# Optimization experiments

Hardware: AMD Instinct MI355X
Metric: run time of the kernel (lower is better)

Reference implementation:

```python
import jax, jax.numpy as jnp
import numpy as np

B, S, D, H = 2, 2048, 1024, 16
DK = D // H  # 64
ROPE_THETA = 10000.0


def apply_rope(t, positions):
    # t: [B, H, S, DK]; positions: [B, S]
    half = DK // 2
    inv_freq = 1.0 / (ROPE_THETA ** (jnp.arange(0, DK, 2, dtype=jnp.float32) / DK))  # [half]
    ang = positions.astype(jnp.float32)[:, None, :, None] * inv_freq  # [B,1,S,half]
    cos, sin = jnp.cos(ang), jnp.sin(ang)
    t_even = t[..., 0::2]
    t_odd = t[..., 1::2]
    r_even = t_even * cos - t_odd * sin
    r_odd = t_even * sin + t_odd * cos
    # interleave back to original layout
    return jnp.stack([r_even, r_odd], axis=-1).reshape(t.shape)


def setup_inputs() -> dict:
    key = jax.random.key(0)
    ks = jax.random.split(key, 5)
    x = jax.random.normal(ks[0], (B, S, D), dtype=jnp.float32)
    token_positions = jnp.broadcast_to(jnp.arange(S, dtype=jnp.int64 if jax.config.jax_enable_x64 else jnp.int32), (B, S))
    w_q = jax.random.normal(ks[1], (D, D), dtype=jnp.float32)
    w_k = jax.random.normal(ks[2], (D, D), dtype=jnp.float32)
    w_v = jax.random.normal(ks[3], (D, D), dtype=jnp.float32)
    w_o = jax.random.normal(ks[4], (D, D), dtype=jnp.float32)
    return {"x": x, "token_positions": token_positions, "w_q": w_q, "w_k": w_k, "w_v": w_v, "w_o": w_o}


def reference(x, token_positions, w_q, w_k, w_v, w_o):
    # project: weights stored as (h*d_k, d_model)
    wq = w_q.reshape(H, DK, D)
    wk = w_k.reshape(H, DK, D)
    wv = w_v.reshape(H, DK, D)
    q = jnp.einsum('bsd,hkd->bhsk', x, wq)  # [B,H,S,DK]
    k = jnp.einsum('bsd,hkd->bhsk', x, wk)
    v = jnp.einsum('bsd,hkd->bhsk', x, wv)
    q = apply_rope(q, token_positions)
    k = apply_rope(k, token_positions)
    scale = 1.0 / jnp.sqrt(jnp.float32(DK))
    scores = jnp.einsum('bhnk,bhmk->bhnm', q, k) * scale  # [B,H,S,S]
    causal = jnp.tril(jnp.ones((S, S), dtype=bool))
    scores = jnp.where(causal, scores, -jnp.inf)
    attn = jax.nn.softmax(scores, axis=-1)
    out = jnp.einsum('bhnm,bhmv->bhnv', attn, v)  # [B,H,S,DK]
    out = jnp.transpose(out, (0, 2, 1, 3)).reshape(B, S, H * DK)
    return jnp.einsum('bsf,df->bsd', out, w_o)
```

## Files before the change

### kernel.cpp

```cpp
#include <hip/hip_runtime.h>

typedef unsigned short u16;
typedef unsigned int u32;
typedef __attribute__((ext_vector_type(8))) __bf16 bf16x8;
typedef __attribute__((ext_vector_type(4))) float f32x4;

#define NSEQ 2048
#define NDIM 1024
#define NHEAD 16
#define NTOK 4096
#define NX   4194304
#define NWEL 1048576

__device__ __forceinline__ u16 f2bf(float f) {
  unsigned u = __float_as_uint(f);
  return (u16)((u + 0x7fffu + ((u >> 16) & 1u)) >> 16);
}
__device__ __forceinline__ float bf2f(u16 h) {
  return __uint_as_float(((unsigned)h) << 16);
}
__device__ __forceinline__ bf16x8 ld16(const u16* p) {
  int4 v = *reinterpret_cast<const int4*>(p);
  return __builtin_bit_cast(bf16x8, v);
}
__device__ __forceinline__ f32x4 mfma16(bf16x8 a, bf16x8 b, f32x4 c) {
  return __builtin_amdgcn_mfma_f32_16x16x32_bf16(a, b, c, 0, 0, 0);
}
__device__ __forceinline__ void gload16(const u16* g, u16* l) {
  __builtin_amdgcn_global_load_lds(
      (const __attribute__((address_space(1))) void*)g,
      (__attribute__((address_space(3))) void*)l, 16, 0, 0);
}

#define GEMM_PROLOGUE                                                         \
  const int tid = threadIdx.x;                                                \
  const int lane = tid & 63, wid = tid >> 6;                                  \
  const int wm = wid >> 1, wn = wid & 1;                                      \
  const int lr = lane & 15, lg = lane >> 4;                                   \
  const int srow_ = tid >> 2;                                                 \
  const int sch_ = ((tid & 3) ^ ((tid >> 3) & 3)) * 8;                        \
  const int rsw_ = (lg ^ ((lr >> 1) & 3)) * 8;

#define STAGE3(BB, AH, AL, BH, BL, T0, J0, K0)                                \
  {                                                                           \
    u16* bb_ = (BB);                                                          \
    gload16(AH + (size_t)((T0) + srow_) * NDIM + (K0) + sch_, bb_ + tid * 8); \
    gload16(AH + (size_t)((T0) + 64 + srow_) * NDIM + (K0) + sch_,            \
            bb_ + 2048 + tid * 8);                                            \
    gload16(BH + (size_t)((J0) + srow_) * NDIM + (K0) + sch_,                 \
            bb_ + 4096 + tid * 8);                                            \
    gload16(BH + (size_t)((J0) + 64 + srow_) * NDIM + (K0) + sch_,            \
            bb_ + 6144 + tid * 8);                                            \
    gload16(AL + (size_t)((T0) + srow_) * NDIM + (K0) + sch_,                 \
            bb_ + 8192 + tid * 8);                                            \
    gload16(AL + (size_t)((T0) + 64 + srow_) * NDIM + (K0) + sch_,            \
            bb_ + 10240 + tid * 8);                                           \
    gload16(BL + (size_t)((J0) + srow_) * NDIM + (K0) + sch_,                 \
            bb_ + 12288 + tid * 8);                                           \
    gload16(BL + (size_t)((J0) + 64 + srow_) * NDIM + (K0) + sch_,            \
            bb_ + 14336 + tid * 8);                                           \
  }

#define GEMM3_LOOP(AH, AL, BH, BL, T0, J0)                                    \
  STAGE3(lds, AH, AL, BH, BL, T0, J0, 0)                                      \
  __syncthreads();                                                            \
  for (int k0 = 0; k0 < NDIM; k0 += 32) {                                     \
    u16* cb_ = lds + ((k0 >> 5) & 1) * 16384;                                 \
    if (k0 + 32 < NDIM) {                                                     \
      u16* nb_ = lds + ((((k0 >> 5) & 1) ^ 1) * 16384);                       \
      STAGE3(nb_, AH, AL, BH, BL, T0, J0, k0 + 32)                            \
    }                                                                         \
    bf16x8 afh[4], afl[4];                                                    \
    _Pragma("unroll") for (int m = 0; m < 4; m++) {                           \
      int off = (wm * 64 + m * 16 + lr) * 32 + rsw_;                          \
      afh[m] = ld16(cb_ + off);                                               \
      afl[m] = ld16(cb_ + 8192 + off);                                        \
    }                                                                         \
    _Pragma("unroll") for (int n = 0; n < 4; n++) {                           \
      int off = (wn * 64 + n * 16 + lr) * 32 + rsw_;                          \
      bf16x8 bfh = ld16(cb_ + 4096 + off);                                    \
      bf16x8 bfl = ld16(cb_ + 12288 + off);                                   \
      _Pragma("unroll") for (int m = 0; m < 4; m++) {                         \
        acc[m][n] = mfma16(afh[m], bfh, acc[m][n]);                           \
        acc[m][n] = mfma16(afh[m], bfl, acc[m][n]);                           \
        acc[m][n] = mfma16(afl[m], bfh, acc[m][n]);                           \
      }                                                                       \
    }                                                                         \
    __syncthreads();                                                          \
  }

#define STAGE1(BB, AH, BH, T0, J0, K0)                                        \
  {                                                                           \
    u16* bb_ = (BB);                                                          \
    gload16(AH + (size_t)((T0) + srow_) * NDIM + (K0) + sch_, bb_ + tid * 8); \
    gload16(AH + (size_t)((T0) + 64 + srow_) * NDIM + (K0) + sch_,            \
            bb_ + 2048 + tid * 8);                                            \
    gload16(BH + (size_t)((J0) + srow_) * NDIM + (K0) + sch_,                 \
            bb_ + 4096 + tid * 8);                                            \
    gload16(BH + (size_t)((J0) + 64 + srow_) * NDIM + (K0) + sch_,            \
            bb_ + 6144 + tid * 8);                                            \
  }

#define GEMM1_LOOP(AH, BH, T0, J0)                                            \
  STAGE1(lds, AH, BH, T0, J0, 0)                                              \
  __syncthreads();                                                            \
  for (int k0 = 0; k0 < NDIM; k0 += 32) {                                     \
    u16* cb_ = lds + ((k0 >> 5) & 1) * 8192;                                  \
    if (k0 + 32 < NDIM) {                                                     \
      u16* nb_ = lds + ((((k0 >> 5) & 1) ^ 1) * 8192);                        \
      STAGE1(nb_, AH, BH, T0, J0, k0 + 32)                                    \
    }                                                                         \
    bf16x8 afh[4];                                                            \
    _Pragma("unroll") for (int m = 0; m < 4; m++) {                           \
      int off = (wm * 64 + m * 16 + lr) * 32 + rsw_;                          \
      afh[m] = ld16(cb_ + off);                                               \
    }                                                                         \
    _Pragma("unroll") for (int n = 0; n < 4; n++) {                           \
      int off = (wn * 64 + n * 16 + lr) * 32 + rsw_;                          \
      bf16x8 bfh = ld16(cb_ + 4096 + off);                                    \
      _Pragma("unroll") for (int m = 0; m < 4; m++) {                         \
        acc[m][n] = mfma16(afh[m], bfh, acc[m][n]);                           \
      }                                                                       \
    }                                                                         \
    __syncthreads();                                                          \
  }

__global__ __launch_bounds__(256) void k_prep(
    const float* __restrict__ x, const float* __restrict__ wq,
    const float* __restrict__ wk, const float* __restrict__ wv,
    const float* __restrict__ wo,
    u16* __restrict__ xh, u16* __restrict__ xl,
    u16* __restrict__ wh, u16* __restrict__ wl) {
  int g = blockIdx.x * 256 + threadIdx.x;
  const float4* src;
  u16 *dh, *dl;
  int idx;
  bool wantlo = true;
  if (g < NX / 4) {
    src = (const float4*)x; dh = xh; dl = xl; idx = g;
  } else {
    int z = (g - NX / 4) / (NWEL / 4);
    int r = (g - NX / 4) % (NWEL / 4);
    src = (const float4*)(z == 0 ? wq : z == 1 ? wk : z == 2 ? wv : wo);
    dh = wh + (size_t)z * NWEL; dl = wl + (size_t)z * NWEL; idx = r;
    wantlo = (z < 2);
  }
  float4 v = src[idx];
  u16 h0 = f2bf(v.x), h1 = f2bf(v.y), h2 = f2bf(v.z), h3 = f2bf(v.w);
  ushort4 hv = make_ushort4(h0, h1, h2, h3);
  ((ushort4*)dh)[idx] = hv;
  if (wantlo) {
    ushort4 lv = make_ushort4(f2bf(v.x - bf2f(h0)), f2bf(v.y - bf2f(h1)),
                              f2bf(v.z - bf2f(h2)), f2bf(v.w - bf2f(h3)));
    ((ushort4*)dl)[idx] = lv;
  }
}

__global__ __launch_bounds__(256) void k_tab(float2* __restrict__ csn) {
  int idx = blockIdx.x * 256 + threadIdx.x;
  int p = idx >> 5, j = idx & 31;
  double invf = exp((double)(2 * j) * (-9.210340371976184 / 64.0));
  double ang = (double)p * invf;
  double kq = rint(ang * 0.15915494309189535);
  float a = (float)(ang - kq * 6.283185307179586);
  csn[idx] = make_float2(cosf(a), sinf(a));
}

__global__ __launch_bounds__(256) void k_qkv(
    const u16* __restrict__ xh, const u16* __restrict__ xl,
    const u16* __restrict__ wh, const u16* __restrict__ wl,
    const int* __restrict__ tokpos, const float2* __restrict__ csn,
    u16* __restrict__ qh, u16* __restrict__ ql,
    u16* __restrict__ kh, u16* __restrict__ kl) {
  __shared__ __align__(16) u16 lds[32768];
  const int z = blockIdx.z;
  const int t0 = blockIdx.y * 128, j0 = blockIdx.x * 128;
  const int h0 = j0 >> 6;
  GEMM_PROLOGUE
  const u16* Bh = wh + (size_t)z * NWEL;
  const u16* Bl = wl + (size_t)z * NWEL;
  f32x4 acc[4][4];
#pragma unroll
  for (int m = 0; m < 4; m++)
#pragma unroll
    for (int n = 0; n < 4; n++) acc[m][n] = f32x4{0.f, 0.f, 0.f, 0.f};
  GEMM3_LOOP(xh, xl, Bh, Bl, t0, j0)

  const int b = t0 >> 11, s0 = t0 & 2047;
  u16* dh = (z == 0) ? qh : kh;
  u16* dl = (z == 0) ? ql : kl;
  float rv[4][4][4];
#pragma unroll
  for (int m = 0; m < 4; m++) {
#pragma unroll
    for (int r = 0; r < 4; r++) {
      int pos = tokpos[t0 + wm * 64 + m * 16 + lg * 4 + r];
#pragma unroll
      for (int n = 0; n < 4; n++) {
        float val = acc[m][n][r];
        float nb = __shfl_xor(val, 1);
        int dk = (wn * 64 + n * 16 + lr) & 63;
        float2 cs = csn[pos * 32 + (dk >> 1)];
        rv[m][r][n] = (dk & 1) ? (nb * cs.y + val * cs.x)
                               : (val * cs.x - nb * cs.y);
      }
    }
  }
#pragma unroll
  for (int pass = 0; pass < 2; pass++) {
    __syncthreads();
#pragma unroll
    for (int m = 0; m < 4; m++)
#pragma unroll
      for (int r = 0; r < 4; r++) {
        int rloc = wm * 64 + m * 16 + lg * 4 + r;
#pragma unroll
        for (int n = 0; n < 4; n++) {
          int cloc = wn * 64 + n * 16 + lr;
          float v = rv[m][r][n];
          u16 hi = f2bf(v);
          lds[rloc * 128 + cloc] = pass == 0 ? hi : f2bf(v - bf2f(hi));
        }
      }
    __syncthreads();
    u16* dst = pass == 0 ? dh : dl;
#pragma unroll
    for (int i = 0; i < 8; i++) {
      int idx = tid + i * 256;
      int r = idx >> 4, cc = idx & 15;
      int4 v = *(int4*)(lds + r * 128 + cc * 8);
      int h2 = cc >> 3, dk = (cc & 7) * 8;
      size_t off = ((size_t)((b * NHEAD + h0 + h2) * NSEQ + s0 + r)) * 64 + dk;
      *(int4*)(dst + off) = v;
    }
  }
}

__global__ __launch_bounds__(256) void k_v(
    const u16* __restrict__ xh, const u16* __restrict__ wvh,
    u16* __restrict__ vt) {
  __shared__ __align__(16) u16 lds[16384];
  const int t0 = blockIdx.y * 128, j0 = blockIdx.x * 128;
  const int h0 = j0 >> 6;
  GEMM_PROLOGUE
  f32x4 acc[4][4];
#pragma unroll
  for (int m = 0; m < 4; m++)
#pragma unroll
    for (int n = 0; n < 4; n++) acc[m][n] = f32x4{0.f, 0.f, 0.f, 0.f};
  GEMM1_LOOP(xh, wvh, t0, j0)
  const int b = t0 >> 11, s0 = t0 & 2047;
#pragma unroll
  for (int m = 0; m < 4; m++)
#pragma unroll
    for (int r = 0; r < 4; r++) {
      int rloc = wm * 64 + m * 16 + lg * 4 + r;
#pragma unroll
      for (int n = 0; n < 4; n++) {
        int cloc = wn * 64 + n * 16 + lr;
        lds[cloc * 128 + (rloc ^ ((cloc & 15) << 3))] = f2bf(acc[m][n][r]);
      }
    }
  __syncthreads();
#pragma unroll
  for (int i = 0; i < 8; i++) {
    int idx = tid + i * 256;
    int col = idx >> 4, rc = idx & 15;
    int4 v = *(int4*)(lds + col * 128 + ((rc * 8) ^ ((col & 15) << 3)));
    int h2 = col >> 6, dk = col & 63;
    size_t off = ((size_t)((b * NHEAD + h0 + h2) * 64 + dk)) * NSEQ + s0 + rc * 8;
    *(int4*)(vt + off) = v;
  }
}

#define ATT_STAGE(SEL, KT)                                                    \
  _Pragma("unroll") for (int j_ = 0; j_ < 6; j_++) {                          \
    int seg_ = w * 6 + j_;                                                    \
    int ten_ = seg_ >> 3, sub_ = seg_ & 7;                                    \
    int row_ = sub_ * 8 + (lane >> 3);                                        \
    int sc_ = ((lane & 7) * 8) ^ ((row_ & 7) * 8);             \
    u16* dst_ = (ten_ == 0 ? &skh[SEL][0]                                     \
                           : ten_ == 1 ? &skl[SEL][0] : &svb[SEL][0]) +       \
                sub_ * 512;                                                   \
    const u16* src_ =                                                         \
        (ten_ == 2)                                                           \
            ? vt + vbase + (size_t)row_ * NSEQ + (KT) * 64 + sc_              \
            : (ten_ == 0 ? kh : kl) + base + (size_t)((KT) * 64 + row_) * 64 + sc_; \
    gload16(src_, dst_);                                                      \
  }

__global__ __launch_bounds__(256) void k_attn(
    const u16* __restrict__ qh, const u16* __restrict__ ql,
    const u16* __restrict__ kh, const u16* __restrict__ kl,
    const u16* __restrict__ vt, u16* __restrict__ ah) {
  __shared__ __align__(16) u16 skh[2][4096];
  __shared__ __align__(16) u16 skl[2][4096];
  __shared__ __align__(16) u16 svb[2][4096];
  __shared__ __align__(16) u16 sp[4096];
  const int tid = threadIdx.x, lane = tid & 63, w = tid >> 6;
  const int lr = lane & 15, lg = lane >> 4;
  const int bh = blockIdx.y;
  const size_t base = (size_t)bh * NSEQ * 64;
  const size_t vbase = (size_t)bh * 64 * NSEQ;
  const int b = bh >> 4, h = bh & 15;
  const int qbA = 31 - blockIdx.x, qbB = blockIdx.x;

  for (int ph = 0; ph < 2; ph++) {
    const int qblk = ph ? qbB : qbA;
    const int q0 = qblk * 64;
    const int nt = qblk + 1;
    const int qrow_g = q0 + w * 16 + lr;
    bf16x8 qfh[2], qfl[2];
#pragma unroll
    for (int kk = 0; kk < 2; kk++) {
      qfh[kk] = ld16(qh + base + (size_t)qrow_g * 64 + kk * 32 + lg * 8);
      qfl[kk] = ld16(ql + base + (size_t)qrow_g * 64 + kk * 32 + lg * 8);
    }
    float mrun = -__builtin_inff(), lrun = 0.f;
    f32x4 oacc[4];
#pragma unroll
    for (int nf = 0; nf < 4; nf++) oacc[nf] = f32x4{0.f, 0.f, 0.f, 0.f};

    int sel = 0;
    ATT_STAGE(0, 0)
    __syncthreads();
    for (int kt = 0; kt < nt; kt++) {
      if (kt + 1 < nt) { ATT_STAGE(sel ^ 1, kt + 1) }
      f32x4 sacc[4];
#pragma unroll
      for (int nf = 0; nf < 4; nf++) sacc[nf] = f32x4{0.f, 0.f, 0.f, 0.f};
#pragma unroll
      for (int nf = 0; nf < 4; nf++) {
        int krow = nf * 16 + lr;
        int swz = (krow & 7) * 8;
#pragma unroll
        for (int kk = 0; kk < 2; kk++) {
          int off = krow * 64 + ((kk * 32 + lg * 8) ^ swz);
          bf16x8 kfh = ld16(&skh[sel][0] + off);
          bf16x8 kfl = ld16(&skl[sel][0] + off);
          sacc[nf] = mfma16(kfh, qfh[kk], sacc[nf]);
          sacc[nf] = mfma16(kfl, qfh[kk], sacc[nf]);
          sacc[nf] = mfma16(kfh, qfl[kk], sacc[nf]);
        }
      }
      float sv[4][4];
      float mm[4];
#pragma unroll
      for (int nf = 0; nf < 4; nf++) {
#pragma unroll
        for (int r = 0; r < 4; r++) sv[nf][r] = sacc[nf][r] * 0.125f;
      }
      if (kt == qblk) {
#pragma unroll
        for (int nf = 0; nf < 4; nf++)
#pragma unroll
          for (int r = 0; r < 4; r++) {
            int colg = kt * 64 + nf * 16 + lg * 4 + r;
            if (colg > qrow_g) sv[nf][r] = -__builtin_inff();
          }
      }
#pragma unroll
      for (int nf = 0; nf < 4; nf++)
        mm[nf] = fmaxf(fmaxf(sv[nf][0], sv[nf][1]), fmaxf(sv[nf][2], sv[nf][3]));
      float rmax = fmaxf(fmaxf(mm[0], mm[1]), fmaxf(mm[2], mm[3]));
      rmax = fmaxf(rmax, __shfl_xor(rmax, 16));
      rmax = fmaxf(rmax, __shfl_xor(rmax, 32));
      float mnew = fmaxf(mrun, rmax);
      float alpha = __expf(mrun - mnew);
      mrun = mnew;
      float p[4][4];
      float ss[4];
#pragma unroll
      for (int nf = 0; nf < 4; nf++) {
#pragma unroll
        for (int r = 0; r < 4; r++) p[nf][r] = __expf(sv[nf][r] - mnew);
        ss[nf] = (p[nf][0] + p[nf][1]) + (p[nf][2] + p[nf][3]);
      }
      float rsum = (ss[0] + ss[1]) + (ss[2] + ss[3]);
      rsum += __shfl_xor(rsum, 16);
      rsum += __shfl_xor(rsum, 32);
      lrun = lrun * alpha + rsum;
      {
        int prow = w * 16 + lr;
        int swz = (prow & 7) * 8;
#pragma unroll
        for (int nf = 0; nf < 4; nf++) {
          u32 w0 = (u32)f2bf(p[nf][0]) | ((u32)f2bf(p[nf][1]) << 16);
          u32 w1 = (u32)f2bf(p[nf][2]) | ((u32)f2bf(p[nf][3]) << 16);
          int col = (nf * 16 + lg * 4) ^ swz;
          *(uint2*)(&sp[prow * 64 + col]) = make_uint2(w0, w1);
        }
      }
      {
        float af0 = __shfl(alpha, lg * 4 + 0);
        float af1 = __shfl(alpha, lg * 4 + 1);
        float af2 = __shfl(alpha, lg * 4 + 2);
        float af3 = __shfl(alpha, lg * 4 + 3);
#pragma unroll
        for (int nf = 0; nf < 4; nf++) {
          oacc[nf][0] *= af0; oacc[nf][1] *= af1;
          oacc[nf][2] *= af2; oacc[nf][3] *= af3;
        }
      }
      {
        int prow = w * 16 + lr;
        int pswz = (prow & 7) * 8;
#pragma unroll
        for (int kk = 0; kk < 2; kk++) {
          bf16x8 pa = ld16(&sp[prow * 64 + ((kk * 32 + lg * 8) ^ pswz)]);
#pragma unroll
          for (int nf = 0; nf < 4; nf++) {
            int vrow = nf * 16 + lr;
            bf16x8 vb = ld16(&svb[sel][0] + vrow * 64 +
                             ((kk * 32 + lg * 8) ^ ((vrow & 7) * 8)));
            oacc[nf] = mfma16(pa, vb, oacc[nf]);
          }
        }
      }
      __syncthreads();
      sel ^= 1;
    }
    float inv = 1.0f / lrun;
    float iv0 = __shfl(inv, lg * 4 + 0);
    float iv1 = __shfl(inv, lg * 4 + 1);
    float iv2 = __shfl(inv, lg * 4 + 2);
    float iv3 = __shfl(inv, lg * 4 + 3);
#pragma unroll
    for (int r = 0; r < 4; r++) {
      float ivr = r == 0 ? iv0 : r == 1 ? iv1 : r == 2 ? iv2 : iv3;
      int row = q0 + w * 16 + lg * 4 + r;
      size_t toff = ((size_t)(b * NSEQ + row)) * NDIM + h * 64;
#pragma unroll
      for (int nf = 0; nf < 4; nf++) {
        ah[toff + nf * 16 + lr] = f2bf(oacc[nf][r] * ivr);
      }
    }
  }
}

__global__ __launch_bounds__(256) void k_out(
    const u16* __restrict__ ah, const u16* __restrict__ wh,
    float* __restrict__ out) {
  __shared__ __align__(16) u16 lds[16384];
  const int t0 = blockIdx.y * 128, j0 = blockIdx.x * 128;
  GEMM_PROLOGUE
  f32x4 acc[4][4];
#pragma unroll
  for (int m = 0; m < 4; m++)
#pragma unroll
    for (int n = 0; n < 4; n++) acc[m][n] = f32x4{0.f, 0.f, 0.f, 0.f};
  GEMM1_LOOP(ah, wh, t0, j0)
#pragma unroll
  for (int m = 0; m < 4; m++)
#pragma unroll
    for (int r = 0; r < 4; r++) {
      int row = t0 + wm * 64 + m * 16 + lg * 4 + r;
#pragma unroll
      for (int n = 0; n < 4; n++) {
        int col = j0 + wn * 64 + n * 16 + lr;
        out[(size_t)row * NDIM + col] = acc[m][n][r];
      }
    }
}

extern "C" void kernel_launch(void* const* d_in, const int* in_sizes, int n_in,
                              void* d_out, int out_size, void* d_ws, size_t ws_size,
                              hipStream_t stream) {
  (void)in_sizes; (void)n_in; (void)out_size; (void)ws_size;
  const float* x = (const float*)d_in[0];
  const int* tokpos = (const int*)d_in[1];
  const float* wq = (const float*)d_in[2];
  const float* wk = (const float*)d_in[3];
  const float* wv = (const float*)d_in[4];
  const float* wo = (const float*)d_in[5];
  float* out = (float*)d_out;

  u16* ws = (u16*)d_ws;
  u16* xh = ws;
  u16* xl = xh + NX;
  u16* wh = xl + NX;
  u16* wl = wh + 4 * (size_t)NWEL;
  u16* qh = wl + 4 * (size_t)NWEL;
  u16* ql = qh + NX;
  u16* kh = ql + NX;
  u16* kl = kh + NX;
  u16* vt = kl + NX;
  float2* csn = (float2*)(vt + NX);

  k_prep<<<dim3(8192), dim3(256), 0, stream>>>(x, wq, wk, wv, wo, xh, xl, wh, wl);
  k_tab<<<dim3(256), dim3(256), 0, stream>>>(csn);
  k_qkv<<<dim3(8, 32, 2), dim3(256), 0, stream>>>(xh, xl, wh, wl, tokpos, csn,
                                                  qh, ql, kh, kl);
  k_v<<<dim3(8, 32), dim3(256), 0, stream>>>(xh, wh + 2 * (size_t)NWEL, vt);
  k_attn<<<dim3(16, 32), dim3(256), 0, stream>>>(qh, ql, kh, kl, vt, xh);
  k_out<<<dim3(8, 32), dim3(256), 0, stream>>>(xh, wh + 3 * (size_t)NWEL, out);
}
```

Before: 179.6 us.

## Add lazy softmax rescale, exp2 scaling, packed bf16 convert, block swizzle, setprio

Folds log2(e) into the score scale so exp2f replaces __expf, and skips the running max update and output rescale unless some row max exceeds the running max by more than 8 (wave-uniform __any). Replaces manual bf16 rounding with the v_cvt_pk_bf16_f32 instruction. Remaps the flat block id so consecutive blocks land on different head groups, and raises wave priority around the MFMA sections. The lazy rescale lets probabilities grow up to 2^8 before renormalising, which trades some headroom against fewer exp and multiply operations.

```diff
diff --git a/kernel.cpp b/kernel.cpp
--- a/kernel.cpp
+++ b/kernel.cpp
@@ -25,6 +25,11 @@
 }
 __device__ __forceinline__ f32x4 mfma16(bf16x8 a, bf16x8 b, f32x4 c) {
   return __builtin_amdgcn_mfma_f32_16x16x32_bf16(a, b, c, 0, 0, 0);
+}
+__device__ __forceinline__ u32 cvtpk(float lo, float hi) {
+  u32 r;
+  asm("v_cvt_pk_bf16_f32 %0, %1, %2" : "=v"(r) : "v"(lo), "v"(hi));
+  return r;
 }
 __device__ __forceinline__ void gload16(const u16* g, u16* l) {
   __builtin_amdgcn_global_load_lds(
@@ -299,11 +304,15 @@
   __shared__ __align__(16) u16 sp[4096];
   const int tid = threadIdx.x, lane = tid & 63, w = tid >> 6;
   const int lr = lane & 15, lg = lane >> 4;
-  const int bh = blockIdx.y;
+  const int fid = blockIdx.y * 16 + blockIdx.x;
+  const int vb_ = (fid & 7) * 64 + (fid >> 3);
+  const int bh = vb_ >> 4;
+  const int qpair = vb_ & 15;
   const size_t base = (size_t)bh * NSEQ * 64;
   const size_t vbase = (size_t)bh * 64 * NSEQ;
   const int b = bh >> 4, h = bh & 15;
-  const int qbA = 31 - blockIdx.x, qbB = blockIdx.x;
+  const int qbA = 31 - qpair, qbB = qpair;
+  const float SC2 = 0.18033688011112042f;
 
   for (int ph = 0; ph < 2; ph++) {
     const int qblk = ph ? qbB : qbA;
@@ -329,6 +338,7 @@
       f32x4 sacc[4];
 #pragma unroll
       for (int nf = 0; nf < 4; nf++) sacc[nf] = f32x4{0.f, 0.f, 0.f, 0.f};
+      __builtin_amdgcn_s_setprio(1);
 #pragma unroll
       for (int nf = 0; nf < 4; nf++) {
         int krow = nf * 16 + lr;
@@ -343,12 +353,12 @@
           sacc[nf] = mfma16(kfh, qfl[kk], sacc[nf]);
         }
       }
-      float sv[4][4];
-      float mm[4];
+      __builtin_amdgcn_s_setprio(0);
+      float sv[4][4], mm[4];
 #pragma unroll
       for (int nf = 0; nf < 4; nf++) {
 #pragma unroll
-        for (int r = 0; r < 4; r++) sv[nf][r] = sacc[nf][r] * 0.125f;
+        for (int r = 0; r < 4; r++) sv[nf][r] = sacc[nf][r] * SC2;
       }
       if (kt == qblk) {
 #pragma unroll
@@ -365,33 +375,38 @@
       float rmax = fmaxf(fmaxf(mm[0], mm[1]), fmaxf(mm[2], mm[3]));
       rmax = fmaxf(rmax, __shfl_xor(rmax, 16));
       rmax = fmaxf(rmax, __shfl_xor(rmax, 32));
-      float mnew = fmaxf(mrun, rmax);
-      float alpha = __expf(mrun - mnew);
-      mrun = mnew;
+      float alpha = 1.f;
+      bool resc = __any(rmax > mrun + 8.f);
+      if (resc) {
+        float mnew = fmaxf(mrun, rmax);
+        alpha = exp2f(mrun - mnew);
+        mrun = mnew;
+        lrun *= alpha;
+      }
       float p[4][4];
       float ss[4];
 #pragma unroll
       for (int nf = 0; nf < 4; nf++) {
 #pragma unroll
-        for (int r = 0; r < 4; r++) p[nf][r] = __expf(sv[nf][r] - mnew);
+        for (int r = 0; r < 4; r++) p[nf][r] = exp2f(sv[nf][r] - mrun);
         ss[nf] = (p[nf][0] + p[nf][1]) + (p[nf][2] + p[nf][3]);
       }
       float rsum = (ss[0] + ss[1]) + (ss[2] + ss[3]);
       rsum += __shfl_xor(rsum, 16);
       rsum += __shfl_xor(rsum, 32);
-      lrun = lrun * alpha + rsum;
+      lrun += rsum;
       {
         int prow = w * 16 + lr;
         int swz = (prow & 7) * 8;
 #pragma unroll
         for (int nf = 0; nf < 4; nf++) {
-          u32 w0 = (u32)f2bf(p[nf][0]) | ((u32)f2bf(p[nf][1]) << 16);
-          u32 w1 = (u32)f2bf(p[nf][2]) | ((u32)f2bf(p[nf][3]) << 16);
+          u32 w0 = cvtpk(p[nf][0], p[nf][1]);
+          u32 w1 = cvtpk(p[nf][2], p[nf][3]);
           int col = (nf * 16 + lg * 4) ^ swz;
           *(uint2*)(&sp[prow * 64 + col]) = make_uint2(w0, w1);
         }
       }
-      {
+      if (resc) {
         float af0 = __shfl(alpha, lg * 4 + 0);
         float af1 = __shfl(alpha, lg * 4 + 1);
         float af2 = __shfl(alpha, lg * 4 + 2);
@@ -405,17 +420,19 @@
       {
         int prow = w * 16 + lr;
         int pswz = (prow & 7) * 8;
+        __builtin_amdgcn_s_setprio(1);
 #pragma unroll
         for (int kk = 0; kk < 2; kk++) {
           bf16x8 pa = ld16(&sp[prow * 64 + ((kk * 32 + lg * 8) ^ pswz)]);
 #pragma unroll
           for (int nf = 0; nf < 4; nf++) {
             int vrow = nf * 16 + lr;
-            bf16x8 vb = ld16(&svb[sel][0] + vrow * 64 +
-                             ((kk * 32 + lg * 8) ^ ((vrow & 7) * 8)));
-            oacc[nf] = mfma16(pa, vb, oacc[nf]);
+            bf16x8 vb2 = ld16(&svb[sel][0] + vrow * 64 +
+                              ((kk * 32 + lg * 8) ^ ((vrow & 7) * 8)));
+            oacc[nf] = mfma16(pa, vb2, oacc[nf]);
           }
         }
+        __builtin_amdgcn_s_setprio(0);
       }
       __syncthreads();
       sel ^= 1;
```

Measured after the change: 179.7 us. No clear change (+0.1%).
